# Performance work log

Hardware: AMD Instinct MI355X
Metric: run time of the kernel (lower is better)

Reference implementation:

```python
import jax, jax.numpy as jnp
import numpy as np

B, T, P = 16, 512, 2048
S_NUM, S_DEN = 256, 1024
DEN_SCALE = 1.0


def setup_inputs() -> dict:
    key = jax.random.key(0)
    ks = jax.random.split(key, 10)
    inp = {
        "input": jax.random.normal(ks[0], (B, T, P), dtype=jnp.float32),
        # lengths in [T//2, T] so every sequence is non-trivial
        "seqlengths": jax.random.randint(ks[1], (B,), T // 2, T + 1),
        "num_init": jax.random.normal(ks[2], (S_NUM,), dtype=jnp.float32),
        "num_trans": jax.nn.log_softmax(jax.random.normal(ks[3], (S_NUM, S_NUM), dtype=jnp.float32), axis=-1),
        "num_final": jax.random.normal(ks[4], (S_NUM,), dtype=jnp.float32),
        "num_pdf": jax.random.randint(ks[5], (S_NUM,), 0, P),
        "den_init": jax.random.normal(ks[6], (S_DEN,), dtype=jnp.float32),
        "den_trans": jax.nn.log_softmax(jax.random.normal(ks[7], (S_DEN, S_DEN), dtype=jnp.float32), axis=-1),
        "den_final": jax.random.normal(ks[8], (S_DEN,), dtype=jnp.float32),
        "den_pdf": jax.random.randint(ks[9], (S_DEN,), 0, P),
    }
    return inp


def _seq_logprob(loglikes, seqlengths, init, trans, final, pdf_ids):
    """Forward-algorithm log-marginal of each sequence under a dense FSM.

    loglikes: [B, T, P] frame pdf log-likelihoods
    Returns [B] log total probabilities.
    """
    emis = loglikes[:, :, pdf_ids]  # [B, T, S] state emissions via pdf gather
    alpha0 = init[None, :] + emis[:, 0, :]  # [B, S]

    def step(alpha, xt):
        t, e_t = xt  # e_t: [B, S]
        # alpha_new[b, s'] = logsumexp_s(alpha[b, s] + trans[s, s']) + e_t[b, s']
        a_new = jax.nn.logsumexp(alpha[:, :, None] + trans[None, :, :], axis=1) + e_t
        # freeze alpha once past each sequence's length
        alpha = jnp.where((t < seqlengths)[:, None], a_new, alpha)
        return alpha, None

    ts = jnp.arange(1, emis.shape[1])
    emis_t = jnp.moveaxis(emis[:, 1:, :], 1, 0)  # [T-1, B, S]
    alphaT, _ = jax.lax.scan(step, alpha0, (ts, emis_t))
    return jax.nn.logsumexp(alphaT + final[None, :], axis=-1)  # [B]


def reference(input, seqlengths, num_init, num_trans, num_final, num_pdf,
              den_init, den_trans, den_final, den_pdf):
    num_llh = jnp.sum(_seq_logprob(input, seqlengths, num_init, num_trans, num_final, num_pdf))
    den_llh = jnp.sum(_seq_logprob(input, seqlengths, den_init, den_trans, den_final, den_pdf))
    return -(num_llh - DEN_SCALE * den_llh)
```

## Files before the change

kernel.cpp:

```cpp
#include <hip/hip_runtime.h>

#define AG __HIP_MEMORY_SCOPE_AGENT
#define B_ 16
#define T_ 512
#define P_ 2048
#define SN_ 256
#define SD_ 1024
#define NGD 8
#define GB 16
#define NBD (NGD * GB)
#define NBLK (NBD + B_)
#define NTHR 1024
#define CHU 136

typedef unsigned long long u64;

__device__ __forceinline__ float alf(const float* p){ return __hip_atomic_load(p, __ATOMIC_RELAXED, AG); }
__device__ __forceinline__ void  asf(float* p, float v){ __hip_atomic_store(p, v, __ATOMIC_RELAXED, AG); }
__device__ __forceinline__ void  rsu(unsigned* p, unsigned v){ __hip_atomic_store(p, v, __ATOMIC_RELEASE, AG); }
__device__ __forceinline__ u64   ald64(const u64* p){ return __hip_atomic_load(p, __ATOMIC_RELAXED, AG); }
__device__ __forceinline__ void  ast64(u64* p, u64 v){ __hip_atomic_store(p, v, __ATOMIC_RELAXED, AG); }
__device__ __forceinline__ u64   pk(float v, unsigned t){ return ((u64)t << 32) | (u64)__float_as_uint(v); }
__device__ __forceinline__ void wait_eq(unsigned* p, unsigned v){
  while (__hip_atomic_load(p, __ATOMIC_RELAXED, AG) != v) __builtin_amdgcn_s_sleep(1);
  asm volatile("" ::: "memory");
}
__device__ __forceinline__ float poll_tag(const u64* p, unsigned et){
  u64 x = ald64(p);
  while ((unsigned)(x >> 32) != et) x = ald64(p);
  return __uint_as_float((unsigned)x);
}

__global__ void __attribute__((amdgpu_flat_work_group_size(1024, 1024)))
__attribute__((amdgpu_waves_per_eu(4, 4))) lfmmi_kernel(
    const float* __restrict__ input, const int* __restrict__ seqlen,
    const float* __restrict__ num_init, const float* __restrict__ num_trans,
    const float* __restrict__ num_final, const int* __restrict__ num_pdf,
    const float* __restrict__ den_init, const float* __restrict__ den_trans,
    const float* __restrict__ den_final, const int* __restrict__ den_pdf,
    float* __restrict__ out, float* __restrict__ ws)
{
  __shared__ __align__(16) unsigned char smem[24832];
  const int tid = threadIdx.x;
  const int bid = blockIdx.x;

  u64*      Qc     = (u64*)ws;
  float*    DenRes = (float*)(Qc + 2*NGD*GB*CHU);
  float*    NumRes = DenRes + 16;
  unsigned* DF     = (unsigned*)(NumRes + 16);
  unsigned* NF     = DF + NGD*16;

  const int wv = tid >> 6, ln = tid & 63;

  if (bid < NBD) {
    const int g = bid >> 4, r = bid & 15;
    const int cg = tid & 31, kq = tid >> 5;
    const int col0 = r * 64;

    float* qs   = (float*)smem;
    float* redA = (float*)(smem + 16384);
    float* redB = redA + 1024;
    float* Ms   = (float*)(smem + 24576);

    float wA[32], wB[32];
    {
      const float* wb = den_trans + (size_t)(kq * 32) * SD_ + col0 + cg;
      #pragma unroll
      for (int kk = 0; kk < 32; ++kk) {
        wA[kk] = __expf(wb[(size_t)kk * SD_]);
        wB[kk] = __expf(wb[(size_t)kk * SD_ + 32]);
      }
    }

    const int b0 = 2 * g, b1 = 2 * g + 1;
    const int slen0 = seqlen[b0], slen1 = seqlen[b1];
    const size_t inb0 = (size_t)b0 * T_ * P_, inb1 = (size_t)b1 * T_ * P_;
    int pdf0 = 0;
    if (wv == 0) pdf0 = den_pdf[col0 + ln];

    if (wv == 0) {
      u64* ch0 = Qc + ((size_t)(0 * NGD + g) * GB + r) * CHU;
      const float v0 = __expf(den_init[col0 + ln] + input[inb0 + pdf0]);
      const float v1 = __expf(den_init[col0 + ln] + input[inb1 + pdf0]);
      ast64(ch0 + ln, pk(v0, 0u)); ast64(ch0 + 64 + ln, pk(v1, 0u));
      if (r == 0) {
        float m0 = v0, m1 = v1;
        #pragma unroll
        for (int d = 1; d < 64; d <<= 1) {
          m0 = fmaxf(m0, __shfl_xor(m0, d));
          m1 = fmaxf(m1, __shfl_xor(m1, d));
        }
        if (ln == 0) { ast64(ch0 + 128, pk(m0, 0u)); ast64(ch0 + 129, pk(m1, 0u)); }
      }
    }

    float Lr0 = 0.f, Lr1 = 0.f;
    for (int t = 1; t <= 511; ++t) {
      const int pp = (t - 1) & 1, pc = t & 1;
      const unsigned et = (unsigned)(t - 1);
      float e0 = 0.f, e1 = 0.f;
      if (wv == 0) {
        e0 = input[inb0 + (size_t)t * P_ + pdf0];
        e1 = input[inb1 + (size_t)t * P_ + pdf0];
      }
      {
        const u64* ch = Qc + ((size_t)(pp * NGD + g) * GB + wv) * CHU;
        qs[pp * 2048 + wv * 64 + ln]        = poll_tag(ch + ln, et);
        qs[pp * 2048 + 1024 + wv * 64 + ln] = poll_tag(ch + 64 + ln, et);
        if (wv == 0 && ln < 2) {
          const u64* mh = Qc + ((size_t)(pp * NGD + g) * GB + 0) * CHU + 128;
          Ms[pp * 2 + ln] = poll_tag(mh + ln, et);
        }
      }
      __syncthreads();
      const float* q0 = qs + pp * 2048 + kq * 32;
      const float* q1 = q0 + 1024;
      float a00 = 0.f, a01 = 0.f, a10 = 0.f, a11 = 0.f;
      #pragma unroll
      for (int jj = 0; jj < 8; ++jj) {
        const float4 f0 = *(const float4*)(q0 + 4 * jj);
        const float4 f1 = *(const float4*)(q1 + 4 * jj);
        a00 = fmaf(f0.x, wA[4*jj+0], a00); a00 = fmaf(f0.y, wA[4*jj+1], a00);
        a00 = fmaf(f0.z, wA[4*jj+2], a00); a00 = fmaf(f0.w, wA[4*jj+3], a00);
        a01 = fmaf(f0.x, wB[4*jj+0], a01); a01 = fmaf(f0.y, wB[4*jj+1], a01);
        a01 = fmaf(f0.z, wB[4*jj+2], a01); a01 = fmaf(f0.w, wB[4*jj+3], a01);
        a10 = fmaf(f1.x, wA[4*jj+0], a10); a10 = fmaf(f1.y, wA[4*jj+1], a10);
        a10 = fmaf(f1.z, wA[4*jj+2], a10); a10 = fmaf(f1.w, wA[4*jj+3], a10);
        a11 = fmaf(f1.x, wB[4*jj+0], a11); a11 = fmaf(f1.y, wB[4*jj+1], a11);
        a11 = fmaf(f1.z, wB[4*jj+2], a11); a11 = fmaf(f1.w, wB[4*jj+3], a11);
      }
      a00 += __shfl_xor(a00, 32); a01 += __shfl_xor(a01, 32);
      a10 += __shfl_xor(a10, 32); a11 += __shfl_xor(a11, 32);
      if (ln < 32) {
        redA[wv * 64 + cg] = a00; redA[wv * 64 + 32 + cg] = a01;
        redB[wv * 64 + cg] = a10; redB[wv * 64 + 32 + cg] = a11;
      }
      __syncthreads();
      if (wv == 0) {
        float acc0 = 0.f, acc1 = 0.f;
        #pragma unroll
        for (int w = 0; w < 16; ++w) {
          acc0 += redA[w * 64 + ln];
          acc1 += redB[w * 64 + ln];
        }
        const float Mv0 = Ms[pp * 2 + 0], Mv1 = Ms[pp * 2 + 1];
        const float v0 = (t < slen0) ? (acc0 / Mv0) * __expf(e0)
                                     : qs[pp * 2048 + col0 + ln];
        const float v1 = (t < slen1) ? (acc1 / Mv1) * __expf(e1)
                                     : qs[pp * 2048 + 1024 + col0 + ln];
        u64* ch = Qc + ((size_t)(pc * NGD + g) * GB + r) * CHU;
        ast64(ch + ln, pk(v0, (unsigned)t));
        ast64(ch + 64 + ln, pk(v1, (unsigned)t));
        if (r == 0) {
          float m0 = v0, m1 = v1;
          #pragma unroll
          for (int d = 1; d < 64; d <<= 1) {
            m0 = fmaxf(m0, __shfl_xor(m0, d));
            m1 = fmaxf(m1, __shfl_xor(m1, d));
          }
          if (ln == 0) {
            ast64(ch + 128, pk(m0, (unsigned)t));
            ast64(ch + 129, pk(m1, (unsigned)t));
            if (t < slen0) Lr0 += __logf(Mv0);
            if (t < slen1) Lr1 += __logf(Mv1);
          }
        }
      }
    }

    if (r == 0) {
      {
        const u64* ch = Qc + ((size_t)(1 * NGD + g) * GB + wv) * CHU;
        qs[2048 + wv * 64 + ln]        = poll_tag(ch + ln, 511u);
        qs[2048 + 1024 + wv * 64 + ln] = poll_tag(ch + 64 + ln, 511u);
      }
      __syncthreads();
      float* red = redA;
      const int b2e = tid >> 9, ce = tid & 511;
      red[tid] = qs[2048 + b2e * 1024 + ce] * __expf(den_final[ce])
               + qs[2048 + b2e * 1024 + 512 + ce] * __expf(den_final[512 + ce]);
      __syncthreads();
      for (int off = 256; off; off >>= 1) {
        const int base = (tid >= 512) ? 512 : 0, i = tid - base;
        if (i < off) red[base + i] += red[base + i + off];
        __syncthreads();
      }
      if (tid == 0) {
        asf(DenRes + 2 * g,     Lr0 + __logf(red[0]));
        asf(DenRes + 2 * g + 1, Lr1 + __logf(red[512]));
        rsu(DF + g * 16, 0x600D0000u | (unsigned)g);
        if (g == 0) {
          for (int g2 = 0; g2 < NGD; ++g2) wait_eq(DF + g2 * 16, 0x600D0000u | (unsigned)g2);
          for (int b2 = 0; b2 < B_; ++b2)  wait_eq(NF + b2 * 16, 0x600D0100u | (unsigned)b2);
          float sden = 0.f, snum = 0.f;
          for (int i = 0; i < 16; ++i) { sden += alf(DenRes + i); snum += alf(NumRes + i); }
          out[0] = -(snum - sden);
        }
      }
    }
  } else {
    const int b = bid - NBD;
    float* qn   = (float*)smem;
    float* redn = (float*)(smem + 2048);
    float* Ms2  = (float*)(smem + 18432);
    const size_t inb = (size_t)b * T_ * P_;
    const int slen = seqlen[b];

    float wn[64];
    {
      const float* wb = num_trans + (size_t)(wv * 16) * SN_ + ln;
      #pragma unroll
      for (int kk = 0; kk < 16; ++kk) {
        #pragma unroll
        for (int cc = 0; cc < 4; ++cc)
          wn[kk * 4 + cc] = __expf(wb[(size_t)kk * SN_ + 64 * cc]);
      }
    }
    int pdfn[4] = {0, 0, 0, 0};
    float Lr = 0.f;
    if (wv == 0) {
      #pragma unroll
      for (int cc = 0; cc < 4; ++cc) pdfn[cc] = num_pdf[ln + 64 * cc];
      float mx = 0.f;
      #pragma unroll
      for (int cc = 0; cc < 4; ++cc) {
        const float v = __expf(num_init[ln + 64 * cc] + input[inb + pdfn[cc]]);
        qn[ln + 64 * cc] = v;
        mx = fmaxf(mx, v);
      }
      #pragma unroll
      for (int d = 1; d < 64; d <<= 1) mx = fmaxf(mx, __shfl_xor(mx, d));
      if (ln == 0) Ms2[0] = mx;
    }
    __syncthreads();

    int tlast = 0;
    for (int t = 1; t <= 511; ++t) {
      if (t >= slen) break;
      tlast = t;
      const int pr = (t - 1) & 1, pw = t & 1;
      float e[4] = {0.f, 0.f, 0.f, 0.f};
      if (wv == 0) {
        #pragma unroll
        for (int cc = 0; cc < 4; ++cc) e[cc] = input[inb + (size_t)t * P_ + pdfn[cc]];
      }
      const float* qp = qn + pr * 256 + wv * 16;
      float ac[4] = {0.f, 0.f, 0.f, 0.f};
      #pragma unroll
      for (int jj = 0; jj < 4; ++jj) {
        const float4 f = *(const float4*)(qp + 4 * jj);
        #pragma unroll
        for (int cc = 0; cc < 4; ++cc) {
          ac[cc] = fmaf(f.x, wn[(4*jj+0)*4+cc], ac[cc]);
          ac[cc] = fmaf(f.y, wn[(4*jj+1)*4+cc], ac[cc]);
          ac[cc] = fmaf(f.z, wn[(4*jj+2)*4+cc], ac[cc]);
          ac[cc] = fmaf(f.w, wn[(4*jj+3)*4+cc], ac[cc]);
        }
      }
      #pragma unroll
      for (int cc = 0; cc < 4; ++cc) redn[wv * 256 + cc * 64 + ln] = ac[cc];
      __syncthreads();
      if (wv == 0) {
        float acc[4] = {0.f, 0.f, 0.f, 0.f};
        #pragma unroll
        for (int w = 0; w < 16; ++w) {
          #pragma unroll
          for (int cc = 0; cc < 4; ++cc) acc[cc] += redn[w * 256 + cc * 64 + ln];
        }
        const float Mv = Ms2[pr];
        const float rM = 1.0f / Mv;
        float mx = 0.f;
        #pragma unroll
        for (int cc = 0; cc < 4; ++cc) {
          const float v = acc[cc] * rM * __expf(e[cc]);
          qn[pw * 256 + ln + 64 * cc] = v;
          mx = fmaxf(mx, v);
        }
        #pragma unroll
        for (int d = 1; d < 64; d <<= 1) mx = fmaxf(mx, __shfl_xor(mx, d));
        if (ln == 0) { Ms2[pw] = mx; Lr += __logf(Mv); }
      }
      __syncthreads();
    }
    const int cur = tlast & 1;
    if (wv == 0) {
      float s = 0.f;
      #pragma unroll
      for (int cc = 0; cc < 4; ++cc)
        s += qn[cur * 256 + ln + 64 * cc] * __expf(num_final[ln + 64 * cc]);
      #pragma unroll
      for (int d = 1; d < 64; d <<= 1) s += __shfl_xor(s, d);
      if (ln == 0) {
        asf(NumRes + b, Lr + __logf(s));
        rsu(NF + b * 16, 0x600D0100u | (unsigned)b);
      }
    }
  }
}

extern "C" void kernel_launch(void* const* d_in, const int* in_sizes, int n_in,
                              void* d_out, int out_size, void* d_ws, size_t ws_size,
                              hipStream_t stream) {
  const float* input     = (const float*)d_in[0];
  const int*   seqlen    = (const int*)  d_in[1];
  const float* num_init  = (const float*)d_in[2];
  const float* num_trans = (const float*)d_in[3];
  const float* num_final = (const float*)d_in[4];
  const int*   num_pdf   = (const int*)  d_in[5];
  const float* den_init  = (const float*)d_in[6];
  const float* den_trans = (const float*)d_in[7];
  const float* den_final = (const float*)d_in[8];
  const int*   den_pdf   = (const int*)  d_in[9];
  float* out = (float*)d_out;
  float* ws  = (float*)d_ws;

  void* args[] = { &input, &seqlen, &num_init, &num_trans, &num_final, &num_pdf,
                   &den_init, &den_trans, &den_final, &den_pdf, &out, &ws };
  hipLaunchCooperativeKernel((void*)lfmmi_kernel, dim3(NBLK), dim3(NTHR),
                             args, 0, stream);
}
```

Baseline: 1.493 ms.

## Restructure denominator block so each wave owns a 64-row k-slice and shares finalisation

Each wave now holds 64 transition weights for its own k-slice, reads only its own chunk of the previous alpha, and writes partial sums to a double-buffered reduction array. This removes one of the two per-step __syncthreads. The final per-state reduction is spread over all 16 waves with groups of 8 lanes using shuffles, and lead lanes keep alpha in registers for frozen sequences. This replaces the single-wave tail that previously summed 16 partials for 128 outputs, shortening the serial critical path at each time step. The trade-off is higher register pressure from 64 weights per thread, and a reused smem buffer that needs an extra barrier before finalisation.

```diff
diff --git a/kernel.cpp b/kernel.cpp
--- a/kernel.cpp
+++ b/kernel.cpp
@@ -40,7 +40,7 @@
     const float* __restrict__ den_final, const int* __restrict__ den_pdf,
     float* __restrict__ out, float* __restrict__ ws)
 {
-  __shared__ __align__(16) unsigned char smem[24832];
+  __shared__ __align__(16) unsigned char smem[25248];
   const int tid = threadIdx.x;
   const int bid = blockIdx.x;
 
@@ -54,140 +54,125 @@
 
   if (bid < NBD) {
     const int g = bid >> 4, r = bid & 15;
-    const int cg = tid & 31, kq = tid >> 5;
     const int col0 = r * 64;
-
-    float* qs   = (float*)smem;
-    float* redA = (float*)(smem + 16384);
-    float* redB = redA + 1024;
-    float* Ms   = (float*)(smem + 24576);
-
-    float wA[32], wB[32];
+    const int tm = ln >> 3, j8 = ln & 7;
+    const int o  = 8 * wv + tm;
+    const int ob = o >> 6, oc = o & 63;
+    const bool lead = (j8 == 0);
+
+    float* qsW = (float*)smem;
+    float* red = (float*)(smem + 8704);
+    float* Ms  = (float*)(smem + 25216);
+
+    float wreg[64];
     {
-      const float* wb = den_trans + (size_t)(kq * 32) * SD_ + col0 + cg;
-      #pragma unroll
-      for (int kk = 0; kk < 32; ++kk) {
-        wA[kk] = __expf(wb[(size_t)kk * SD_]);
-        wB[kk] = __expf(wb[(size_t)kk * SD_ + 32]);
-      }
+      const float* wb = den_trans + (size_t)(64 * wv) * SD_ + col0 + ln;
+      #pragma unroll
+      for (int j = 0; j < 64; ++j) wreg[j] = __expf(wb[(size_t)j * SD_]);
     }
 
     const int b0 = 2 * g, b1 = 2 * g + 1;
-    const int slen0 = seqlen[b0], slen1 = seqlen[b1];
     const size_t inb0 = (size_t)b0 * T_ * P_, inb1 = (size_t)b1 * T_ * P_;
-    int pdf0 = 0;
-    if (wv == 0) pdf0 = den_pdf[col0 + ln];
-
-    if (wv == 0) {
-      u64* ch0 = Qc + ((size_t)(0 * NGD + g) * GB + r) * CHU;
-      const float v0 = __expf(den_init[col0 + ln] + input[inb0 + pdf0]);
-      const float v1 = __expf(den_init[col0 + ln] + input[inb1 + pdf0]);
-      ast64(ch0 + ln, pk(v0, 0u)); ast64(ch0 + 64 + ln, pk(v1, 0u));
-      if (r == 0) {
-        float m0 = v0, m1 = v1;
-        #pragma unroll
-        for (int d = 1; d < 64; d <<= 1) {
-          m0 = fmaxf(m0, __shfl_xor(m0, d));
-          m1 = fmaxf(m1, __shfl_xor(m1, d));
-        }
-        if (ln == 0) { ast64(ch0 + 128, pk(m0, 0u)); ast64(ch0 + 129, pk(m1, 0u)); }
-      }
-    }
-
-    float Lr0 = 0.f, Lr1 = 0.f;
+    int pdfc = 0, slenL = 0; size_t inbL = 0;
+    if (lead) {
+      pdfc  = den_pdf[col0 + oc];
+      inbL  = ob ? inb1 : inb0;
+      slenL = seqlen[ob ? b1 : b0];
+    }
+    u64* myCh0 = Qc + ((size_t)(0 * NGD + g) * GB + r) * CHU;
+    u64* myCh1 = Qc + ((size_t)(1 * NGD + g) * GB + r) * CHU;
+
+    float v_prev = 0.f, Lr = 0.f;
+    if (lead) {
+      v_prev = __expf(den_init[col0 + oc] + input[inbL + pdfc]);
+      ast64(myCh0 + o, pk(v_prev, 0u));
+    }
+    if (r == 0 && (wv == 0 || wv == 8)) {
+      float mx = lead ? v_prev : 0.f;
+      #pragma unroll
+      for (int d = 1; d < 64; d <<= 1) mx = fmaxf(mx, __shfl_xor(mx, d));
+      if (ln == 0) ast64(myCh0 + 128 + ob, pk(mx, 0u));
+    }
+
     for (int t = 1; t <= 511; ++t) {
       const int pp = (t - 1) & 1, pc = t & 1;
       const unsigned et = (unsigned)(t - 1);
-      float e0 = 0.f, e1 = 0.f;
-      if (wv == 0) {
-        e0 = input[inb0 + (size_t)t * P_ + pdf0];
-        e1 = input[inb1 + (size_t)t * P_ + pdf0];
-      }
+      float e = 0.f;
+      if (lead) e = input[inbL + (size_t)t * P_ + pdfc];
+
       {
-        const u64* ch = Qc + ((size_t)(pp * NGD + g) * GB + wv) * CHU;
-        qs[pp * 2048 + wv * 64 + ln]        = poll_tag(ch + ln, et);
-        qs[pp * 2048 + 1024 + wv * 64 + ln] = poll_tag(ch + 64 + ln, et);
+        const u64* chs = Qc + ((size_t)(pp * NGD + g) * GB + wv) * CHU;
+        const float q0v = poll_tag(chs + ln, et);
+        const float q1v = poll_tag(chs + 64 + ln, et);
+        qsW[wv * 136 + ln]      = q0v;
+        qsW[wv * 136 + 64 + ln] = q1v;
         if (wv == 0 && ln < 2) {
           const u64* mh = Qc + ((size_t)(pp * NGD + g) * GB + 0) * CHU + 128;
           Ms[pp * 2 + ln] = poll_tag(mh + ln, et);
         }
       }
-      __syncthreads();
-      const float* q0 = qs + pp * 2048 + kq * 32;
-      const float* q1 = q0 + 1024;
-      float a00 = 0.f, a01 = 0.f, a10 = 0.f, a11 = 0.f;
-      #pragma unroll
-      for (int jj = 0; jj < 8; ++jj) {
-        const float4 f0 = *(const float4*)(q0 + 4 * jj);
-        const float4 f1 = *(const float4*)(q1 + 4 * jj);
-        a00 = fmaf(f0.x, wA[4*jj+0], a00); a00 = fmaf(f0.y, wA[4*jj+1], a00);
-        a00 = fmaf(f0.z, wA[4*jj+2], a00); a00 = fmaf(f0.w, wA[4*jj+3], a00);
-        a01 = fmaf(f0.x, wB[4*jj+0], a01); a01 = fmaf(f0.y, wB[4*jj+1], a01);
-        a01 = fmaf(f0.z, wB[4*jj+2], a01); a01 = fmaf(f0.w, wB[4*jj+3], a01);
-        a10 = fmaf(f1.x, wA[4*jj+0], a10); a10 = fmaf(f1.y, wA[4*jj+1], a10);
-        a10 = fmaf(f1.z, wA[4*jj+2], a10); a10 = fmaf(f1.w, wA[4*jj+3], a10);
-        a11 = fmaf(f1.x, wB[4*jj+0], a11); a11 = fmaf(f1.y, wB[4*jj+1], a11);
-        a11 = fmaf(f1.z, wB[4*jj+2], a11); a11 = fmaf(f1.w, wB[4*jj+3], a11);
-      }
-      a00 += __shfl_xor(a00, 32); a01 += __shfl_xor(a01, 32);
-      a10 += __shfl_xor(a10, 32); a11 += __shfl_xor(a11, 32);
-      if (ln < 32) {
-        redA[wv * 64 + cg] = a00; redA[wv * 64 + 32 + cg] = a01;
-        redB[wv * 64 + cg] = a10; redB[wv * 64 + 32 + cg] = a11;
-      }
-      __syncthreads();
-      if (wv == 0) {
-        float acc0 = 0.f, acc1 = 0.f;
-        #pragma unroll
-        for (int w = 0; w < 16; ++w) {
-          acc0 += redA[w * 64 + ln];
-          acc1 += redB[w * 64 + ln];
-        }
-        const float Mv0 = Ms[pp * 2 + 0], Mv1 = Ms[pp * 2 + 1];
-        const float v0 = (t < slen0) ? (acc0 / Mv0) * __expf(e0)
-                                     : qs[pp * 2048 + col0 + ln];
-        const float v1 = (t < slen1) ? (acc1 / Mv1) * __expf(e1)
-                                     : qs[pp * 2048 + 1024 + col0 + ln];
-        u64* ch = Qc + ((size_t)(pc * NGD + g) * GB + r) * CHU;
-        ast64(ch + ln, pk(v0, (unsigned)t));
-        ast64(ch + 64 + ln, pk(v1, (unsigned)t));
-        if (r == 0) {
-          float m0 = v0, m1 = v1;
-          #pragma unroll
-          for (int d = 1; d < 64; d <<= 1) {
-            m0 = fmaxf(m0, __shfl_xor(m0, d));
-            m1 = fmaxf(m1, __shfl_xor(m1, d));
-          }
-          if (ln == 0) {
-            ast64(ch + 128, pk(m0, (unsigned)t));
-            ast64(ch + 129, pk(m1, (unsigned)t));
-            if (t < slen0) Lr0 += __logf(Mv0);
-            if (t < slen1) Lr1 += __logf(Mv1);
-          }
+      float a0 = 0.f, a1 = 0.f;
+      {
+        const float* qp = qsW + wv * 136;
+        #pragma unroll
+        for (int jj = 0; jj < 16; ++jj) {
+          const float4 f0 = *(const float4*)(qp + 4 * jj);
+          const float4 f1 = *(const float4*)(qp + 64 + 4 * jj);
+          a0 = fmaf(f0.x, wreg[4*jj+0], a0); a0 = fmaf(f0.y, wreg[4*jj+1], a0);
+          a0 = fmaf(f0.z, wreg[4*jj+2], a0); a0 = fmaf(f0.w, wreg[4*jj+3], a0);
+          a1 = fmaf(f1.x, wreg[4*jj+0], a1); a1 = fmaf(f1.y, wreg[4*jj+1], a1);
+          a1 = fmaf(f1.z, wreg[4*jj+2], a1); a1 = fmaf(f1.w, wreg[4*jj+3], a1);
+        }
+      }
+      red[(pc * 16 + wv) * 129 + ln]      = a0;
+      red[(pc * 16 + wv) * 129 + 64 + ln] = a1;
+      __syncthreads();
+
+      float acc = red[(pc * 16 + 2 * j8) * 129 + o]
+                + red[(pc * 16 + 2 * j8 + 1) * 129 + o];
+      acc += __shfl_xor(acc, 1);
+      acc += __shfl_xor(acc, 2);
+      acc += __shfl_xor(acc, 4);
+      u64* myCh = pc ? myCh1 : myCh0;
+      if (lead) {
+        const float Mv = Ms[pp * 2 + ob];
+        if (t < slenL) v_prev = (acc / Mv) * __expf(e);
+        ast64(myCh + o, pk(v_prev, (unsigned)t));
+      }
+      if (r == 0 && (wv == 0 || wv == 8)) {
+        float mx = lead ? v_prev : 0.f;
+        #pragma unroll
+        for (int d = 1; d < 64; d <<= 1) mx = fmaxf(mx, __shfl_xor(mx, d));
+        if (ln == 0) {
+          ast64(myCh + 128 + ob, pk(mx, (unsigned)t));
+          if (t < slenL) Lr += __logf(Ms[pp * 2 + ob]);
         }
       }
     }
 
     if (r == 0) {
+      __syncthreads();
+      float* qf = (float*)smem;
+      float* rs = (float*)(smem + 8192);
       {
         const u64* ch = Qc + ((size_t)(1 * NGD + g) * GB + wv) * CHU;
-        qs[2048 + wv * 64 + ln]        = poll_tag(ch + ln, 511u);
-        qs[2048 + 1024 + wv * 64 + ln] = poll_tag(ch + 64 + ln, 511u);
-      }
-      __syncthreads();
-      float* red = redA;
+        qf[wv * 64 + ln]        = poll_tag(ch + ln, 511u);
+        qf[1024 + wv * 64 + ln] = poll_tag(ch + 64 + ln, 511u);
+      }
+      __syncthreads();
       const int b2e = tid >> 9, ce = tid & 511;
-      red[tid] = qs[2048 + b2e * 1024 + ce] * __expf(den_final[ce])
-               + qs[2048 + b2e * 1024 + 512 + ce] * __expf(den_final[512 + ce]);
+      rs[tid] = qf[b2e * 1024 + ce] * __expf(den_final[ce])
+              + qf[b2e * 1024 + 512 + ce] * __expf(den_final[512 + ce]);
       __syncthreads();
       for (int off = 256; off; off >>= 1) {
         const int base = (tid >= 512) ? 512 : 0, i = tid - base;
-        if (i < off) red[base + i] += red[base + i + off];
+        if (i < off) rs[base + i] += rs[base + i + off];
         __syncthreads();
       }
+      if (tid == 0)   asf(DenRes + 2 * g,     Lr + __logf(rs[0]));
+      if (tid == 512) asf(DenRes + 2 * g + 1, Lr + __logf(rs[512]));
+      __syncthreads();
       if (tid == 0) {
-        asf(DenRes + 2 * g,     Lr0 + __logf(red[0]));
-        asf(DenRes + 2 * g + 1, Lr1 + __logf(red[512]));
         rsu(DF + g * 16, 0x600D0000u | (unsigned)g);
         if (g == 0) {
           for (int g2 = 0; g2 < NGD; ++g2) wait_eq(DF + g2 * 16, 0x600D0000u | (unsigned)g2);
```

Measured after the change: 1.398 ms. 1.07x faster.
